# Kernel optimization log

Measured on AMD Instinct MI355X. Metric: run time of the kernel, lower is better.

Reference implementation:

```python
import jax, jax.numpy as jnp
import numpy as np

N_NODES = 50000
N_EDGES = 800000
IN_CH = 128
OUT_CH = 32
HEADS = 4
NEG_SLOPE = 0.2


def setup_inputs() -> dict:
    key = jax.random.key(0)
    k = jax.random.split(key, 6)
    x = jax.random.normal(k[0], (N_NODES, IN_CH), dtype=jnp.float32)
    edge_index = jax.random.randint(k[1], (2, N_EDGES), 0, N_NODES, dtype=jnp.int32)
    # Glorot-style init for the learned parameters of GATConv
    W = jax.random.normal(k[2], (IN_CH, HEADS * OUT_CH), dtype=jnp.float32) / np.sqrt(IN_CH)
    att_src = jax.random.normal(k[3], (HEADS, OUT_CH), dtype=jnp.float32) / np.sqrt(OUT_CH)
    att_dst = jax.random.normal(k[4], (HEADS, OUT_CH), dtype=jnp.float32) / np.sqrt(OUT_CH)
    bias = jnp.zeros((HEADS * OUT_CH,), dtype=jnp.float32)
    return {"x": x, "edge_index": edge_index, "W": W,
            "att_src": att_src, "att_dst": att_dst, "bias": bias}


def reference(x, edge_index, W, att_src, att_dst, bias):
    # PyG GATConv, single layer: concat=True, add_self_loops=True, neg_slope=0.2
    N = x.shape[0]
    H, C = att_src.shape
    # add self loops (PyG default)
    loop = jnp.arange(N, dtype=edge_index.dtype)
    src = jnp.concatenate([edge_index[0], loop])  # [E+N] message sources j
    dst = jnp.concatenate([edge_index[1], loop])  # [E+N] message targets i
    # linear projection per head
    h = (x @ W).reshape(N, H, C)                  # [N,H,C]
    a_src = jnp.einsum('nhc,hc->nh', h, att_src)  # [N,H]
    a_dst = jnp.einsum('nhc,hc->nh', h, att_dst)  # [N,H]
    # edge-wise attention logits with LeakyReLU
    e = jax.nn.leaky_relu(a_src[src] + a_dst[dst], NEG_SLOPE)  # [E',H]
    # segment softmax over incoming edges of each destination node
    m = jax.ops.segment_max(e, dst, num_segments=N)            # [N,H]
    expe = jnp.exp(e - m[dst])
    denom = jax.ops.segment_sum(expe, dst, num_segments=N)     # [N,H]
    alpha = expe / denom[dst]                                  # [E',H]
    # scatter-aggregate weighted messages
    out = jax.ops.segment_sum(h[src] * alpha[:, :, None], dst, num_segments=N)  # [N,H,C]
    return out.reshape(N, H * C) + bias
```

## Files before the change

kernel.cpp:

```cpp
#include <hip/hip_runtime.h>


constexpr int N_NODES = 50000;
constexpr int N_EDGES = 800000;
constexpr int HC      = 128;
constexpr float NEG_SLOPE = 0.2f;
constexpr int M_TILES = N_NODES / 16;
constexpr int NB_PASSA = 256;
constexpr int NB_GEMM  = 512;
constexpr int EPB      = N_EDGES / NB_PASSA;
constexpr int BIN      = 64;
constexpr int NBKT     = 64;
constexpr int BW       = 782;
constexpr int CAP      = 96;
constexpr int LDA      = 136;

typedef short short8 __attribute__((ext_vector_type(8)));
typedef float f32x4  __attribute__((ext_vector_type(4)));

__device__ inline unsigned short f2bf(float f) {
    unsigned int u = __float_as_uint(f);
    u += 0x7FFF + ((u >> 16) & 1);
    return (unsigned short)(u >> 16);
}


__global__ __launch_bounds__(256) void gemm_passA(
    const float* __restrict__ x,
    const float* __restrict__ W,
    const float* __restrict__ att_src, const float* __restrict__ att_dst,
    const int* __restrict__ esrc, const int* __restrict__ edst,
    unsigned short* __restrict__ hb,
    float* __restrict__ a_src, float* __restrict__ a_dst,
    unsigned int* __restrict__ seg,
    int* __restrict__ seg_cnt)
{
    __shared__ int cnt_l[NBKT];
    __shared__ unsigned short As[2][16][LDA];
    if (blockIdx.x < NB_PASSA) {
        const int p = blockIdx.x;
        if (threadIdx.x < NBKT) cnt_l[threadIdx.x] = 0;
        __syncthreads();
        const int e0 = p * EPB, e1 = e0 + EPB;
        for (int e = e0 + threadIdx.x; e < e1; e += 256) {
            const int d = edst[e];
            const int s = esrc[e];
            const int b = d / BW;
            const int pos = atomicAdd(&cnt_l[b], 1);
            if (pos < CAP)
                seg[((p * NBKT) + b) * CAP + pos] =
                    ((unsigned int)s << 10) | (unsigned int)(d - b * BW);
        }
        __syncthreads();
        if (threadIdx.x < NBKT)
            seg_cnt[p * NBKT + threadIdx.x] = min(cnt_l[threadIdx.x], CAP);
        return;
    }
    const int tid  = threadIdx.x;
    const int wave = tid >> 6;
    const int lane = tid & 63;
    const int n0   = (wave & 1) * 64;
    const int l15  = lane & 15;
    const int quad = lane >> 4;

    short8 bfrag[4][4];
    #pragma unroll
    for (int t = 0; t < 4; ++t)
        #pragma unroll
        for (int ks = 0; ks < 4; ++ks) {
            short8 b;
            #pragma unroll
            for (int j = 0; j < 8; ++j)
                b[j] = (short)f2bf(W[(ks * 32 + quad * 8 + j) * 128 + n0 + t * 16 + l15]);
            bfrag[t][ks] = b;
        }

    float asw[4], adw[4];
    #pragma unroll
    for (int t = 0; t < 4; ++t) {
        asw[t] = att_src[n0 + t * 16 + l15];
        adw[t] = att_dst[n0 + t * 16 + l15];
    }

    const int gb = blockIdx.x - NB_PASSA;
    for (int mtb = gb * 2; mtb < M_TILES; mtb += NB_GEMM * 2) {
        #pragma unroll
        for (int j = 0; j < 4; ++j) {
            const int g   = tid + j * 256;
            const int tl  = g >> 9;
            const int w   = g & 511;
            const int row = w >> 5;
            const int c4  = w & 31;
            const int mts = mtb + tl;
            if (mts < M_TILES) {
                const float4 u = *(const float4*)&x[(size_t)(mts * 16 + row) * 128 + c4 * 4];
                ushort4 v;
                v.x = f2bf(u.x); v.y = f2bf(u.y); v.z = f2bf(u.z); v.w = f2bf(u.w);
                *(ushort4*)&As[tl][row][c4 * 4] = v;
            }
        }
        __syncthreads();

        const int mt = mtb + (wave >> 1);
        if (mt < M_TILES) {
            const int m0 = mt * 16;
            const int tl = wave >> 1;

            short8 afrag[4];
            #pragma unroll
            for (int ks = 0; ks < 4; ++ks)
                afrag[ks] = *(const short8*)&As[tl][l15][ks * 32 + quad * 8];

            f32x4 acc[4];
            #pragma unroll
            for (int t = 0; t < 4; ++t) acc[t] = (f32x4){0.f, 0.f, 0.f, 0.f};

            #pragma unroll
            for (int ks = 0; ks < 4; ++ks)
                #pragma unroll
                for (int t = 0; t < 4; ++t)
                    acc[t] = __builtin_amdgcn_mfma_f32_16x16x32_bf16(afrag[ks], bfrag[t][ks], acc[t], 0, 0, 0);

            #pragma unroll
            for (int t = 0; t < 4; ++t)
                #pragma unroll
                for (int r = 0; r < 4; ++r)
                    hb[(m0 + quad * 4 + r) * 128 + n0 + t * 16 + l15] = f2bf(acc[t][r]);

            float hs[2][4] = {{0.f,0.f,0.f,0.f},{0.f,0.f,0.f,0.f}};
            float hd[2][4] = {{0.f,0.f,0.f,0.f},{0.f,0.f,0.f,0.f}};
            #pragma unroll
            for (int t = 0; t < 4; ++t)
                #pragma unroll
                for (int r = 0; r < 4; ++r) {
                    hs[t >> 1][r] += acc[t][r] * asw[t];
                    hd[t >> 1][r] += acc[t][r] * adw[t];
                }
            #pragma unroll
            for (int off = 1; off < 16; off <<= 1)
                #pragma unroll
                for (int g = 0; g < 2; ++g)
                    #pragma unroll
                    for (int r = 0; r < 4; ++r) {
                        hs[g][r] += __shfl_xor(hs[g][r], off);
                        hd[g][r] += __shfl_xor(hd[g][r], off);
                    }
            if (l15 == 0) {
                const int hb0 = n0 >> 5;
                #pragma unroll
                for (int g = 0; g < 2; ++g)
                    #pragma unroll
                    for (int r = 0; r < 4; ++r) {
                        a_src[(m0 + quad * 4 + r) * 4 + hb0 + g] = hs[g][r];
                        a_dst[(m0 + quad * 4 + r) * 4 + hb0 + g] = hd[g][r];
                    }
            }
        }
        __syncthreads();
    }
}


__global__ __launch_bounds__(256) void passB(
    const unsigned int* __restrict__ seg, const int* __restrict__ seg_cnt,
    int* __restrict__ deg, unsigned short* __restrict__ csr_bin)
{
    __shared__ unsigned short bin_l[BW * BIN];
    __shared__ int deg_l[BW];
    const int b   = blockIdx.x;
    const int tid = threadIdx.x;
    const int nb  = min(BW, N_NODES - b * BW);

    for (int i = tid; i < BW; i += 256) deg_l[i] = 0;
    __syncthreads();

    const int cnt = seg_cnt[tid * NBKT + b];
    const uint4* s4 = (const uint4*)&seg[((size_t)(tid * NBKT) + b) * CAP];
    for (int i = 0; i < cnt; i += 4) {
        const uint4 u = s4[i >> 2];
        const int rem = cnt - i;
        {
            const int pos = atomicAdd(&deg_l[u.x & 1023u], 1);
            if (pos < BIN - 1) bin_l[(u.x & 1023u) * BIN + 1 + pos] = (unsigned short)(u.x >> 10);
        }
        if (rem > 1) {
            const int pos = atomicAdd(&deg_l[u.y & 1023u], 1);
            if (pos < BIN - 1) bin_l[(u.y & 1023u) * BIN + 1 + pos] = (unsigned short)(u.y >> 10);
        }
        if (rem > 2) {
            const int pos = atomicAdd(&deg_l[u.z & 1023u], 1);
            if (pos < BIN - 1) bin_l[(u.z & 1023u) * BIN + 1 + pos] = (unsigned short)(u.z >> 10);
        }
        if (rem > 3) {
            const int pos = atomicAdd(&deg_l[u.w & 1023u], 1);
            if (pos < BIN - 1) bin_l[(u.w & 1023u) * BIN + 1 + pos] = (unsigned short)(u.w >> 10);
        }
    }
    __syncthreads();

    uint4* dst = (uint4*)(csr_bin + (size_t)b * BW * BIN);
    const uint4* srcl = (const uint4*)bin_l;
    const int nvec = nb * BIN / 8;
    for (int k = tid; k < nvec; k += 256) dst[k] = srcl[k];
    for (int i = tid; i < nb; i += 256) deg[b * BW + i] = deg_l[i];
}


__global__ __launch_bounds__(256) void gat_agg(
    const int* __restrict__ deg, const unsigned short* __restrict__ csr_bin,
    const unsigned short* __restrict__ hb, const float* __restrict__ a_src,
    const float* __restrict__ a_dst, const float* __restrict__ bias,
    float* __restrict__ out)
{
    __shared__ float ws[4][256];
    const int wv = threadIdx.x >> 6;
    const int node = blockIdx.x * 4 + wv;
    if (node >= N_NODES) return;
    const int lane = threadIdx.x & 63;
    const int q    = lane >> 4;
    const int li   = lane & 15;
    const int ch0  = li * 8;
    const int hd   = li >> 2;
    const float4 ad4 = *(const float4*)&a_dst[node * 4];
    int m = deg[node] + 1;
    if (m > BIN) m = BIN;

    int sv = 0;
    if (lane < m)
        sv = (lane == 0) ? node : (int)csr_bin[(size_t)node * BIN + lane];
    if (lane < m) {
        const float4 av = *(const float4*)&a_src[sv * 4];
        float t; float4 w4;
        t = av.x + ad4.x; t = t > 0.f ? t : NEG_SLOPE * t; w4.x = __expf(t);
        t = av.y + ad4.y; t = t > 0.f ? t : NEG_SLOPE * t; w4.y = __expf(t);
        t = av.z + ad4.z; t = t > 0.f ? t : NEG_SLOPE * t; w4.z = __expf(t);
        t = av.w + ad4.w; t = t > 0.f ? t : NEG_SLOPE * t; w4.w = __expf(t);
        *(float4*)&ws[wv][lane * 4] = w4;
    }

    float acc[8] = {0.f,0.f,0.f,0.f,0.f,0.f,0.f,0.f};
    float dsum = 0.f;

    const int i0 = (q < m) ? q : 0;
    uint4 hv = *(const uint4*)&hb[(size_t)__shfl(sv, i0) * 128 + ch0];
    for (int j = 0; j < m; j += 4) {
        const int ei  = j + q;
        const int idx = ei < m ? ei : j;
        const int ein = ei + 4;
        const int idxn = ein < m ? ein : 0;
        const int s_nxt = __shfl(sv, idxn);
        const uint4 hvn = *(const uint4*)&hb[(size_t)s_nxt * 128 + ch0];
        float w = ws[wv][idx * 4 + hd];
        if (ei >= m) w = 0.f;
        acc[0] += w * __uint_as_float(hv.x << 16);
        acc[1] += w * __uint_as_float(hv.x & 0xFFFF0000u);
        acc[2] += w * __uint_as_float(hv.y << 16);
        acc[3] += w * __uint_as_float(hv.y & 0xFFFF0000u);
        acc[4] += w * __uint_as_float(hv.z << 16);
        acc[5] += w * __uint_as_float(hv.z & 0xFFFF0000u);
        acc[6] += w * __uint_as_float(hv.w << 16);
        acc[7] += w * __uint_as_float(hv.w & 0xFFFF0000u);
        dsum += w;
        hv = hvn;
    }

    #pragma unroll
    for (int off = 16; off <= 32; off <<= 1) {
        #pragma unroll
        for (int r = 0; r < 8; ++r) acc[r] += __shfl_xor(acc[r], off);
        dsum += __shfl_xor(dsum, off);
    }
    if (q == 0) {
        const float inv = 1.f / dsum;
        const float4 b0 = *(const float4*)&bias[ch0];
        const float4 b1 = *(const float4*)&bias[ch0 + 4];
        float4 o0, o1;
        o0.x = acc[0]*inv + b0.x; o0.y = acc[1]*inv + b0.y;
        o0.z = acc[2]*inv + b0.z; o0.w = acc[3]*inv + b0.w;
        o1.x = acc[4]*inv + b1.x; o1.y = acc[5]*inv + b1.y;
        o1.z = acc[6]*inv + b1.z; o1.w = acc[7]*inv + b1.w;
        *(float4*)&out[(size_t)node * HC + ch0]     = o0;
        *(float4*)&out[(size_t)node * HC + ch0 + 4] = o1;
    }
}

extern "C" void kernel_launch(void* const* d_in, const int* in_sizes, int n_in,
                              void* d_out, int out_size, void* d_ws, size_t ws_size,
                              hipStream_t stream) {
    const float* x       = (const float*)d_in[0];
    const int*   ei      = (const int*)  d_in[1];
    const float* W       = (const float*)d_in[2];
    const float* att_src = (const float*)d_in[3];
    const float* att_dst = (const float*)d_in[4];
    const float* bias    = (const float*)d_in[5];
    float* out = (float*)d_out;

    char* p = (char*)d_ws;
    unsigned short* hb  = (unsigned short*)p; p += (size_t)N_NODES * HC * 2;
    float* a_src = (float*)p; p += (size_t)N_NODES * 4 * 4;
    float* a_dst = (float*)p; p += (size_t)N_NODES * 4 * 4;
    unsigned short* csr_bin = (unsigned short*)p; p += (size_t)NBKT * BW * BIN * 2;
    int* deg     = (int*)p;   p += N_NODES * 4;
    unsigned int* seg = (unsigned int*)p; p += (size_t)NB_PASSA * NBKT * CAP * 4;
    int* seg_cnt = (int*)p;   p += NB_PASSA * NBKT * 4;

    const int* esrc = ei;
    const int* edst = ei + N_EDGES;

    gemm_passA<<<NB_PASSA + NB_GEMM, 256, 0, stream>>>(x, W, att_src, att_dst,
                                                       esrc, edst, hb, a_src, a_dst,
                                                       seg, seg_cnt);
    passB     <<<NBKT, 256, 0, stream>>>(seg, seg_cnt, deg, csr_bin);
    gat_agg   <<<(N_NODES + 3) / 4, 256, 0, stream>>>(deg, csr_bin, hb, a_src,
                                                      a_dst, bias, out);
}
```

Before: 147.0 us.

## Bucket CSR neighbor lists by source-node range in passB for gather locality

passB now makes two passes over each destination's incoming edges. The first counts edges per (destination, source-octant) with shared atomics, then an exclusive prefix sum gives per-octant offsets, and the second pass places sources at those offsets. Each destination's neighbor list ends up roughly sorted by source range, so the later gather of source features in gat_agg should have better cache locality. The cost is an extra read of the segment data, a larger shared array that may reduce occupancy, and extra atomics and integer divides.

```diff
diff --git a/kernel.cpp b/kernel.cpp
--- a/kernel.cpp
+++ b/kernel.cpp
@@ -14,6 +14,7 @@
 constexpr int BW       = 782;
 constexpr int CAP      = 96;
 constexpr int LDA      = 136;
+constexpr int NOCT     = 8;
 
 typedef short short8 __attribute__((ext_vector_type(8)));
 typedef float f32x4  __attribute__((ext_vector_type(4)));
@@ -167,33 +168,61 @@
 {
     __shared__ unsigned short bin_l[BW * BIN];
     __shared__ int deg_l[BW];
+    __shared__ int oct_l[BW * NOCT];
     const int b   = blockIdx.x;
     const int tid = threadIdx.x;
     const int nb  = min(BW, N_NODES - b * BW);
 
-    for (int i = tid; i < BW; i += 256) deg_l[i] = 0;
+    for (int i = tid; i < BW * NOCT; i += 256) oct_l[i] = 0;
     __syncthreads();
 
     const int cnt = seg_cnt[tid * NBKT + b];
     const uint4* s4 = (const uint4*)&seg[((size_t)(tid * NBKT) + b) * CAP];
+
+    for (int i = 0; i < cnt; i += 4) {
+        const uint4 u = s4[i >> 2];
+        const int rem = cnt - i;
+        atomicAdd(&oct_l[(u.x & 1023u) * NOCT + (u.x >> 10) / 6250u], 1);
+        if (rem > 1) atomicAdd(&oct_l[(u.y & 1023u) * NOCT + (u.y >> 10) / 6250u], 1);
+        if (rem > 2) atomicAdd(&oct_l[(u.z & 1023u) * NOCT + (u.z >> 10) / 6250u], 1);
+        if (rem > 3) atomicAdd(&oct_l[(u.w & 1023u) * NOCT + (u.w >> 10) / 6250u], 1);
+    }
+    __syncthreads();
+
+    for (int nd = tid; nd < BW; nd += 256) {
+        int s = 0;
+        #pragma unroll
+        for (int k = 0; k < NOCT; ++k) {
+            const int c = oct_l[nd * NOCT + k];
+            oct_l[nd * NOCT + k] = s;
+            s += c;
+        }
+        deg_l[nd] = s;
+    }
+    __syncthreads();
+
     for (int i = 0; i < cnt; i += 4) {
         const uint4 u = s4[i >> 2];
         const int rem = cnt - i;
         {
-            const int pos = atomicAdd(&deg_l[u.x & 1023u], 1);
-            if (pos < BIN - 1) bin_l[(u.x & 1023u) * BIN + 1 + pos] = (unsigned short)(u.x >> 10);
+            const int doff = (int)(u.x & 1023u); const int src = (int)(u.x >> 10);
+            const int pos = atomicAdd(&oct_l[doff * NOCT + src / 6250u], 1);
+            if (pos < BIN - 1) bin_l[doff * BIN + 1 + pos] = (unsigned short)src;
         }
         if (rem > 1) {
-            const int pos = atomicAdd(&deg_l[u.y & 1023u], 1);
-            if (pos < BIN - 1) bin_l[(u.y & 1023u) * BIN + 1 + pos] = (unsigned short)(u.y >> 10);
+            const int doff = (int)(u.y & 1023u); const int src = (int)(u.y >> 10);
+            const int pos = atomicAdd(&oct_l[doff * NOCT + src / 6250u], 1);
+            if (pos < BIN - 1) bin_l[doff * BIN + 1 + pos] = (unsigned short)src;
         }
         if (rem > 2) {
-            const int pos = atomicAdd(&deg_l[u.z & 1023u], 1);
-            if (pos < BIN - 1) bin_l[(u.z & 1023u) * BIN + 1 + pos] = (unsigned short)(u.z >> 10);
+            const int doff = (int)(u.z & 1023u); const int src = (int)(u.z >> 10);
+            const int pos = atomicAdd(&oct_l[doff * NOCT + src / 6250u], 1);
+            if (pos < BIN - 1) bin_l[doff * BIN + 1 + pos] = (unsigned short)src;
         }
         if (rem > 3) {
-            const int pos = atomicAdd(&deg_l[u.w & 1023u], 1);
-            if (pos < BIN - 1) bin_l[(u.w & 1023u) * BIN + 1 + pos] = (unsigned short)(u.w >> 10);
+            const int doff = (int)(u.w & 1023u); const int src = (int)(u.w >> 10);
+            const int pos = atomicAdd(&oct_l[doff * NOCT + src / 6250u], 1);
+            if (pos < BIN - 1) bin_l[doff * BIN + 1 + pos] = (unsigned short)src;
         }
     }
     __syncthreads();
```

Result: slower. 151.6 us (+3.1%).
